# Kernel tuning notes

Hardware: AMD Instinct MI355X
Metric: run time of the kernel (lower is better)

The kernel has to match this reference:

```python
import jax, jax.numpy as jnp
import numpy as np

B, L, D = 1, 1024, 1024
NL = 4            # n_layers
N = 16            # d_state
DI = 2 * D        # d_inner (expand=2)
DTR = (D + 15) // 16  # dt_rank = ceil(d_model/16) = 64
K = 4             # depthwise conv kernel size
EPS = 1e-5


def setup_inputs() -> dict:
    key = jax.random.key(0)
    ks = jax.random.split(key, 8)
    s = lambda k, shp, sc: jax.random.normal(k, shp, jnp.float32) * sc
    x = s(ks[0], (B, L, D), 1.0)
    norm_w = jnp.ones((NL, D), jnp.float32)
    in_w = s(ks[1], (NL, 2 * DI, D), D ** -0.5)          # in_proj (no bias)
    conv_w = s(ks[2], (NL, DI, K), 0.5)                   # depthwise conv1d weight
    conv_b = s(ks[3], (NL, DI), 0.02)                     # conv1d bias
    xproj_w = s(ks[4], (NL, DTR + 2 * N, DI), DI ** -0.5) # x_proj (no bias)
    dt_w = s(ks[5], (NL, DI, DTR), DTR ** -0.5)           # dt_proj weight
    dt_b = jnp.full((NL, DI), 0.1, jnp.float32)           # dt_proj bias (positive-ish delta)
    A_log = jnp.log(jnp.tile(jnp.arange(1, N + 1, dtype=jnp.float32), (NL, DI, 1)))  # [NL, DI, N]
    D_skip = jnp.ones((NL, DI), jnp.float32)
    out_w = s(ks[6], (NL, D, DI), DI ** -0.5)             # out_proj (no bias)
    return dict(x=x, norm_w=norm_w, in_w=in_w, conv_w=conv_w, conv_b=conv_b,
                xproj_w=xproj_w, dt_w=dt_w, dt_b=dt_b, A_log=A_log,
                D_skip=D_skip, out_w=out_w)


def _rmsnorm(x, w):
    return x * jax.lax.rsqrt(jnp.mean(x * x, axis=-1, keepdims=True) + EPS) * w


def _causal_depthwise_conv(u, w, b):
    # u: [B, L, DI], w: [DI, K], b: [DI]; causal (left pad K-1)
    up = jnp.pad(u, ((0, 0), (K - 1, 0), (0, 0)))
    y = b
    for k in range(K):
        y = y + up[:, k:k + L, :] * w[:, k]
    return y


def _selective_scan(dA, dBu, C):
    # dA, dBu: [B, L, DI, N]; C: [B, L, N]
    def step(h, inp):
        a, bu, c = inp
        h = a * h + bu                       # [B, DI, N]
        y = jnp.einsum('bdn,bn->bd', h, c)   # [B, DI]
        return h, y
    h0 = jnp.zeros((dA.shape[0], DI, N), dA.dtype)
    _, ys = jax.lax.scan(step, h0, (dA.transpose(1, 0, 2, 3),
                                    dBu.transpose(1, 0, 2, 3),
                                    C.transpose(1, 0, 2)))
    return ys.transpose(1, 0, 2)             # [B, L, DI]


def _mamba_block(x, p):
    norm_w, in_w, conv_w, conv_b, xproj_w, dt_w, dt_b, A_log, D_skip, out_w = p
    xn = _rmsnorm(x, norm_w)
    xz = jnp.einsum('bld,ed->ble', xn, in_w)             # [B, L, 2*DI]
    u, z = jnp.split(xz, 2, axis=-1)
    u = jax.nn.silu(_causal_depthwise_conv(u, conv_w, conv_b))
    x_dbl = jnp.einsum('bld,ed->ble', u, xproj_w)        # [B, L, DTR+2N]
    dt_r, Bt, Ct = jnp.split(x_dbl, [DTR, DTR + N], axis=-1)
    delta = jax.nn.softplus(jnp.einsum('blr,dr->bld', dt_r, dt_w) + dt_b)  # [B, L, DI]
    A = -jnp.exp(A_log)                                  # [DI, N]
    dA = jnp.exp(delta[..., None] * A)                   # [B, L, DI, N]
    dBu = delta[..., None] * Bt[:, :, None, :] * u[..., None]
    y = _selective_scan(dA, dBu, Ct) + u * D_skip        # [B, L, DI]
    y = y * jax.nn.silu(z)
    return x + jnp.einsum('ble,de->bld', y, out_w)       # residual


def reference(x, norm_w, in_w, conv_w, conv_b, xproj_w, dt_w, dt_b, A_log, D_skip, out_w):
    params = (norm_w, in_w, conv_w, conv_b, xproj_w, dt_w, dt_b, A_log, D_skip, out_w)
    out, _ = jax.lax.scan(lambda h, p: (_mamba_block(h, p), None), x, params)
    return out
```

## Files before the change

### kernel.cpp

```cpp
#include <hip/hip_runtime.h>
#include <hip/hip_bf16.h>
#include <stdint.h>

#define L 1024
#define D 1024
#define NLAYER 4
#define NSTATE 16
#define DI 2048
#define DTR 64
#define KCONV 4
#define XD 96
#define NC 64
#define CT 16
#define KSPLIT 16
#define OSPLIT 4
#define BK 32
#define DIST 4

typedef __attribute__((ext_vector_type(8))) short short8;
typedef __attribute__((ext_vector_type(4))) float floatx4;

__device__ __forceinline__ float siluf(float x) { return x / (1.f + __expf(-x)); }

__device__ __forceinline__ unsigned short f2bf(float x) {
    __hip_bfloat16 b = __float2bfloat16(x);
    return *reinterpret_cast<unsigned short*>(&b);
}

__device__ __forceinline__ short8 pack8(floatx4 a, floatx4 b) {
    short8 o;
    o[0] = (short)f2bf(a.x); o[1] = (short)f2bf(a.y);
    o[2] = (short)f2bf(a.z); o[3] = (short)f2bf(a.w);
    o[4] = (short)f2bf(b.x); o[5] = (short)f2bf(b.y);
    o[6] = (short)f2bf(b.z); o[7] = (short)f2bf(b.w);
    return o;
}

#define BARRIER_NODRAIN() asm volatile("s_waitcnt lgkmcnt(0)\n\ts_barrier" ::: "memory")

template <bool COPYOUT>
__global__ __launch_bounds__(256) void rmsnorm_kernel(const float* __restrict__ x,
                                                      const float* __restrict__ w,
                                                      __hip_bfloat16* __restrict__ xn,
                                                      float* __restrict__ outcpy) {
    int row = blockIdx.x;
    const float* xr = x + (size_t)row * D;
    float v[4];
    float s = 0.f;
#pragma unroll
    for (int i = 0; i < 4; ++i) {
        v[i] = xr[threadIdx.x + i * 256];
        s += v[i] * v[i];
    }
#pragma unroll
    for (int off = 32; off > 0; off >>= 1) s += __shfl_xor(s, off, 64);
    __shared__ float red[4];
    int wave = threadIdx.x >> 6;
    if ((threadIdx.x & 63) == 0) red[wave] = s;
    __syncthreads();
    float tot = red[0] + red[1] + red[2] + red[3];
    float inv = rsqrtf(tot * (1.f / D) + 1e-5f);
#pragma unroll
    for (int i = 0; i < 4; ++i) {
        int c = threadIdx.x + i * 256;
        xn[(size_t)row * D + c] = __float2bfloat16(v[i] * inv * w[c]);
        if (COPYOUT) outcpy[(size_t)row * D + c] = v[i];
    }
}

template <int EPI, int ITERS, bool AF32, int QD>
__global__ __launch_bounds__(256, 2) void gemm_pipe(
    const void* __restrict__ Aptr, int lda,
    const float* __restrict__ Bw, int ldb, int Brows,
    float* __restrict__ C, int ldc, int Nvalid,
    const float* __restrict__ bias) {
    __shared__ __align__(16) __hip_bfloat16 As[2][128 * BK];
    __shared__ __align__(16) __hip_bfloat16 Bs[2][64 * BK];
    int tid = threadIdx.x;
    int wave = tid >> 6, lane = tid & 63;

    int gxy = gridDim.x * gridDim.y;
    int total = gxy * gridDim.z;
    int flat = (blockIdx.z * gridDim.y + blockIdx.y) * gridDim.x + blockIdx.x;
    int bm, bn, bz;
    if ((total & 7) == 0) {
        int lid = (flat & 7) * (total >> 3) + (flat >> 3);
        bz = lid / gxy;
        int rem = lid - bz * gxy;
        bn = rem / gridDim.y;
        bm = rem - bn * gridDim.y;
    } else {
        bm = blockIdx.y; bn = blockIdx.x; bz = blockIdx.z;
    }

    int m0 = bm * 128, n0 = bn * 64;
    int k_base = bz * (ITERS * BK);
    int wr = wave >> 1, wc = wave & 1;
    int srow = lane >> 2, scol = (lane & 3) * 8;
    int q = lane >> 4, r = lane & 15;

    floatx4 acc[4][2] = {};

    int arow0 = m0 + wave * 32 + srow;
    const __hip_bfloat16* gA0 = nullptr; const __hip_bfloat16* gA1 = nullptr;
    const float* gAf0 = nullptr; const float* gAf1 = nullptr;
    if (AF32) {
        gAf0 = (const float*)Aptr + (long)arow0 * lda + scol + k_base;
        gAf1 = gAf0 + (long)16 * lda;
    } else {
        gA0 = (const __hip_bfloat16*)Aptr + (long)arow0 * lda + scol + k_base;
        gA1 = gA0 + (long)16 * lda;
    }
    int bnrow = n0 + wave * 16 + srow;
    const float* gB = Bw + (long)bnrow * ldb + scol + k_base;
    bool bok = bnrow < Brows;

    short8 qa0[QD], qa1[QD];
    floatx4 qaf[AF32 ? QD : 1][4];
    floatx4 qb0[QD] = {}, qb1[QD] = {};

    auto ld = [&](int j) {
        int k0 = j * BK;
        int s = j & (QD - 1);
        if (AF32) {
            qaf[s][0] = *(const floatx4*)(gAf0 + k0);
            qaf[s][1] = *(const floatx4*)(gAf0 + k0 + 4);
            qaf[s][2] = *(const floatx4*)(gAf1 + k0);
            qaf[s][3] = *(const floatx4*)(gAf1 + k0 + 4);
        } else {
            qa0[s] = *(const short8*)(gA0 + k0);
            qa1[s] = *(const short8*)(gA1 + k0);
        }
        if (bok) {
            qb0[s] = *(const floatx4*)(gB + k0);
            qb1[s] = *(const floatx4*)(gB + k0 + 4);
        }
    };
    auto wrstage = [&](int j) {
        int p = j & 1, s = j & (QD - 1);
        if (AF32) {
            *(short8*)(&As[p][(wave * 32 + srow) * BK + scol]) = pack8(qaf[s][0], qaf[s][1]);
            *(short8*)(&As[p][(wave * 32 + 16 + srow) * BK + scol]) = pack8(qaf[s][2], qaf[s][3]);
        } else {
            *(short8*)(&As[p][(wave * 32 + srow) * BK + scol]) = qa0[s];
            *(short8*)(&As[p][(wave * 32 + 16 + srow) * BK + scol]) = qa1[s];
        }
        *(short8*)(&Bs[p][(wave * 16 + srow) * BK + scol]) = pack8(qb0[s], qb1[s]);
    };

#pragma unroll
    for (int j = 0; j < QD; ++j)
        if (j < ITERS) ld(j);
    wrstage(0);

#pragma unroll
    for (int k = 0; k < ITERS; ++k) {
        BARRIER_NODRAIN();
        if (k + QD < ITERS) ld(k + QD);
        if (k + 1 < ITERS) wrstage(k + 1);
        const short* Ap = (const short*)As[k & 1];
        const short* Bp = (const short*)Bs[k & 1];
        short8 af[4], bfr[2];
#pragma unroll
        for (int i = 0; i < 4; ++i)
            af[i] = *(const short8*)(Ap + (wr * 64 + i * 16 + r) * BK + q * 8);
#pragma unroll
        for (int j = 0; j < 2; ++j)
            bfr[j] = *(const short8*)(Bp + (wc * 32 + j * 16 + r) * BK + q * 8);
#pragma unroll
        for (int i = 0; i < 4; ++i)
#pragma unroll
            for (int j = 0; j < 2; ++j)
                acc[i][j] = __builtin_amdgcn_mfma_f32_16x16x32_bf16(af[i], bfr[j], acc[i][j], 0, 0, 0);
    }

#pragma unroll
    for (int i = 0; i < 4; ++i) {
        int mrow = m0 + wr * 64 + i * 16 + q * 4;
#pragma unroll
        for (int j = 0; j < 2; ++j) {
            int ncol = n0 + wc * 32 + j * 16 + r;
            if (ncol < Nvalid) {
#pragma unroll
                for (int rr = 0; rr < 4; ++rr) {
                    float v = acc[i][j][rr];
                    int m = mrow + rr;
                    if (EPI == 1) {
                        v += bias[ncol];
                        v = v > 20.f ? v : log1pf(__expf(v));
                    }
                    if (EPI == 2) atomicAdd(&C[(long)m * ldc + ncol], v);
                    else C[(long)m * ldc + ncol] = v;
                }
            }
        }
    }
}

template <int ITERS, int EPI>
__global__ __launch_bounds__(256, 1) void gemm128(
    const __hip_bfloat16* __restrict__ A, int lda,
    const float* __restrict__ Bw, int ldb, int Brows,
    float* __restrict__ C, int ldc) {
    __shared__ __align__(16) __hip_bfloat16 As[2][128 * BK];
    __shared__ __align__(16) __hip_bfloat16 Bs[2][128 * BK];
    int tid = threadIdx.x;
    int wave = tid >> 6, lane = tid & 63;

    int gxy = gridDim.x * gridDim.y;
    int total = gxy * gridDim.z;
    int flat = (blockIdx.z * gridDim.y + blockIdx.y) * gridDim.x + blockIdx.x;
    int bm, bn, bz;
    if ((total & 7) == 0) {
        int lid = (flat & 7) * (total >> 3) + (flat >> 3);
        bz = lid / gxy;
        int rem = lid - bz * gxy;
        bn = rem / gridDim.y;
        bm = rem - bn * gridDim.y;
    } else {
        bm = blockIdx.y; bn = blockIdx.x; bz = blockIdx.z;
    }

    int m0 = bm * 128, n0 = bn * 128;
    int k_base = bz * (ITERS * BK);
    int wr = wave >> 1, wc = wave & 1;
    int srow = lane >> 2, scol = (lane & 3) * 8;
    int q = lane >> 4, r = lane & 15;

    floatx4 acc[4][4] = {};

    const __hip_bfloat16* gA0 = A + (long)(m0 + wave * 32 + srow) * lda + scol + k_base;
    const __hip_bfloat16* gA1 = gA0 + (long)16 * lda;
    int bn0 = n0 + wave * 32 + srow;
    const float* gB0 = Bw + (long)bn0 * ldb + scol + k_base;
    const float* gB1 = gB0 + (long)16 * ldb;
    bool bok0 = bn0 < Brows, bok1 = (bn0 + 16) < Brows;

    short8 qa0[DIST], qa1[DIST];
    floatx4 qb0[DIST] = {}, qb1[DIST] = {}, qb2[DIST] = {}, qb3[DIST] = {};

    auto ld = [&](int j) {
        int k0 = j * BK;
        int s = j & (DIST - 1);
        qa0[s] = *(const short8*)(gA0 + k0);
        qa1[s] = *(const short8*)(gA1 + k0);
        if (bok0) {
            qb0[s] = *(const floatx4*)(gB0 + k0);
            qb1[s] = *(const floatx4*)(gB0 + k0 + 4);
        }
        if (bok1) {
            qb2[s] = *(const floatx4*)(gB1 + k0);
            qb3[s] = *(const floatx4*)(gB1 + k0 + 4);
        }
    };
    auto wrstage = [&](int j) {
        int p = j & 1, s = j & (DIST - 1);
        *(short8*)(&As[p][(wave * 32 + srow) * BK + scol]) = qa0[s];
        *(short8*)(&As[p][(wave * 32 + 16 + srow) * BK + scol]) = qa1[s];
        *(short8*)(&Bs[p][(wave * 32 + srow) * BK + scol]) = pack8(qb0[s], qb1[s]);
        *(short8*)(&Bs[p][(wave * 32 + 16 + srow) * BK + scol]) = pack8(qb2[s], qb3[s]);
    };

#pragma unroll
    for (int j = 0; j < DIST; ++j)
        if (j < ITERS) ld(j);
    wrstage(0);

#pragma unroll
    for (int k = 0; k < ITERS; ++k) {
        BARRIER_NODRAIN();
        if (k + DIST < ITERS) ld(k + DIST);
        if (k + 1 < ITERS) wrstage(k + 1);
        const short* Ap = (const short*)As[k & 1];
        const short* Bp = (const short*)Bs[k & 1];
        short8 af[4], bfr[4];
#pragma unroll
        for (int i = 0; i < 4; ++i)
            af[i] = *(const short8*)(Ap + (wr * 64 + i * 16 + r) * BK + q * 8);
#pragma unroll
        for (int j = 0; j < 4; ++j)
            bfr[j] = *(const short8*)(Bp + (wc * 64 + j * 16 + r) * BK + q * 8);
#pragma unroll
        for (int i = 0; i < 4; ++i)
#pragma unroll
            for (int j = 0; j < 4; ++j)
                acc[i][j] = __builtin_amdgcn_mfma_f32_16x16x32_bf16(af[i], bfr[j], acc[i][j], 0, 0, 0);
    }

#pragma unroll
    for (int i = 0; i < 4; ++i) {
        int mrow = m0 + wr * 64 + i * 16 + q * 4;
#pragma unroll
        for (int j = 0; j < 4; ++j) {
            int ncol = n0 + wc * 64 + j * 16 + r;
#pragma unroll
            for (int rr = 0; rr < 4; ++rr) {
                if (EPI == 2) atomicAdd(&C[(long)(mrow + rr) * ldc + ncol], acc[i][j][rr]);
                else C[(long)(mrow + rr) * ldc + ncol] = acc[i][j][rr];
            }
        }
    }
}

__global__ __launch_bounds__(256) void conv_silu_kernel(const float* __restrict__ xz,
                                                        const float* __restrict__ cw,
                                                        const float* __restrict__ cb,
                                                        __hip_bfloat16* __restrict__ u,
                                                        float* __restrict__ xdbl96) {
    int idx = blockIdx.x * 256 + threadIdx.x;
    if (blockIdx.x < (L * XD) / 256) xdbl96[idx] = 0.f;
    int d = idx & (DI - 1);
    int t = idx >> 11;
    float acc = cb[d];
#pragma unroll
    for (int k = 0; k < KCONV; ++k) {
        int tk = t - (KCONV - 1) + k;
        if (tk >= 0) acc += xz[(size_t)tk * (2 * DI) + d] * cw[d * KCONV + k];
    }
    u[idx] = __float2bfloat16(siluf(acc));
}

__global__ __launch_bounds__(256) void scanA_kernel(const float* __restrict__ delta,
                                                    const __hip_bfloat16* __restrict__ u,
                                                    const float* __restrict__ xdbl96,
                                                    const float* __restrict__ Alog,
                                                    float* __restrict__ Ach,
                                                    float* __restrict__ Bch) {
    int d = blockIdx.x * 256 + threadIdx.x;
    int c = blockIdx.y;
    __shared__ __align__(16) float Bsh[CT * NSTATE];
    int tt0 = threadIdx.x >> 4, c0 = threadIdx.x & 15;
    Bsh[threadIdx.x] = xdbl96[(size_t)(c * CT + tt0) * XD + DTR + c0];
    __syncthreads();

    float aval[NSTATE];
    const float4* Al4 = (const float4*)(Alog + (size_t)d * NSTATE);
#pragma unroll
    for (int n4 = 0; n4 < 4; ++n4) {
        float4 t = Al4[n4];
        aval[n4 * 4 + 0] = -__expf(t.x);
        aval[n4 * 4 + 1] = -__expf(t.y);
        aval[n4 * 4 + 2] = -__expf(t.z);
        aval[n4 * 4 + 3] = -__expf(t.w);
    }
    float h[NSTATE], ap[NSTATE];
#pragma unroll
    for (int n = 0; n < NSTATE; ++n) { h[n] = 0.f; ap[n] = 1.f; }

    for (int tt = 0; tt < CT; ++tt) {
        int t = c * CT + tt;
        float dl = delta[(size_t)t * DI + d];
        float uu = __bfloat162float(u[(size_t)t * DI + d]);
        float du = dl * uu;
        const float4* Bv = (const float4*)(Bsh + tt * NSTATE);
#pragma unroll
        for (int n4 = 0; n4 < 4; ++n4) {
            float4 b = Bv[n4];
            float bb[4] = {b.x, b.y, b.z, b.w};
#pragma unroll
            for (int k = 0; k < 4; ++k) {
                int n = n4 * 4 + k;
                float a = __expf(dl * aval[n]);
                h[n] = a * h[n] + du * bb[k];
                ap[n] *= a;
            }
        }
    }
    float4* Ao = (float4*)(Ach + ((size_t)c * DI + d) * NSTATE);
    float4* Bo = (float4*)(Bch + ((size_t)c * DI + d) * NSTATE);
#pragma unroll
    for (int n4 = 0; n4 < 4; ++n4) {
        Ao[n4] = make_float4(ap[n4 * 4], ap[n4 * 4 + 1], ap[n4 * 4 + 2], ap[n4 * 4 + 3]);
        Bo[n4] = make_float4(h[n4 * 4], h[n4 * 4 + 1], h[n4 * 4 + 2], h[n4 * 4 + 3]);
    }
}

__global__ __launch_bounds__(256) void scanB_kernel(float* __restrict__ Ach,
                                                    const float* __restrict__ Bch) {
    long i = blockIdx.x * 256 + threadIdx.x;
    const long S = (long)DI * NSTATE;
    constexpr int P = 8;
    float ab[P], bb[P];
#pragma unroll
    for (int j = 0; j < P; ++j) {
        ab[j] = Ach[(long)j * S + i];
        bb[j] = Bch[(long)j * S + i];
    }
    float h = 0.f;
#pragma unroll
    for (int c = 0; c < NC; ++c) {
        float a = ab[c & (P - 1)];
        float b = bb[c & (P - 1)];
        Ach[(long)c * S + i] = h;
        if (c + P < NC) {
            ab[c & (P - 1)] = Ach[(long)(c + P) * S + i];
            bb[c & (P - 1)] = Bch[(long)(c + P) * S + i];
        }
        h = a * h + b;
    }
}

__global__ __launch_bounds__(256) void scanC_kernel(const float* __restrict__ delta,
                                                    const __hip_bfloat16* __restrict__ u,
                                                    const float* __restrict__ xdbl96,
                                                    const float* __restrict__ Alog,
                                                    const float* __restrict__ Hin,
                                                    const float* __restrict__ xz,
                                                    const float* __restrict__ Dskip,
                                                    __hip_bfloat16* __restrict__ yg) {
    int d = blockIdx.x * 256 + threadIdx.x;
    int c = blockIdx.y;
    __shared__ __align__(16) float Bsh[CT * NSTATE];
    __shared__ __align__(16) float Csh[CT * NSTATE];
    int tt0 = threadIdx.x >> 4, c0 = threadIdx.x & 15;
    Bsh[threadIdx.x] = xdbl96[(size_t)(c * CT + tt0) * XD + DTR + c0];
    Csh[threadIdx.x] = xdbl96[(size_t)(c * CT + tt0) * XD + DTR + 16 + c0];
    __syncthreads();

    float aval[NSTATE];
    const float4* Al4 = (const float4*)(Alog + (size_t)d * NSTATE);
#pragma unroll
    for (int n4 = 0; n4 < 4; ++n4) {
        float4 t = Al4[n4];
        aval[n4 * 4 + 0] = -__expf(t.x);
        aval[n4 * 4 + 1] = -__expf(t.y);
        aval[n4 * 4 + 2] = -__expf(t.z);
        aval[n4 * 4 + 3] = -__expf(t.w);
    }
    float h[NSTATE];
    const float4* Hi = (const float4*)(Hin + ((size_t)c * DI + d) * NSTATE);
#pragma unroll
    for (int n4 = 0; n4 < 4; ++n4) {
        float4 t = Hi[n4];
        h[n4 * 4 + 0] = t.x; h[n4 * 4 + 1] = t.y; h[n4 * 4 + 2] = t.z; h[n4 * 4 + 3] = t.w;
    }
    float dsk = Dskip[d];

    for (int tt = 0; tt < CT; ++tt) {
        int t = c * CT + tt;
        float dl = delta[(size_t)t * DI + d];
        float uu = __bfloat162float(u[(size_t)t * DI + d]);
        float du = dl * uu;
        const float4* Bv = (const float4*)(Bsh + tt * NSTATE);
        const float4* Cv = (const float4*)(Csh + tt * NSTATE);
        float y = 0.f;
#pragma unroll
        for (int n4 = 0; n4 < 4; ++n4) {
            float4 b = Bv[n4];
            float4 cc = Cv[n4];
            float bb[4] = {b.x, b.y, b.z, b.w};
            float cv[4] = {cc.x, cc.y, cc.z, cc.w};
#pragma unroll
            for (int k = 0; k < 4; ++k) {
                int n = n4 * 4 + k;
                float a = __expf(dl * aval[n]);
                h[n] = a * h[n] + du * bb[k];
                y += h[n] * cv[k];
            }
        }
        float z = xz[(size_t)t * (2 * DI) + DI + d];
        yg[(size_t)t * DI + d] = __float2bfloat16((y + uu * dsk) * siluf(z));
    }
}

extern "C" void kernel_launch(void* const* d_in, const int* in_sizes, int n_in,
                              void* d_out, int out_size, void* d_ws, size_t ws_size,
                              hipStream_t stream) {
    const float* x      = (const float*)d_in[0];
    const float* norm_w = (const float*)d_in[1];
    const float* in_w   = (const float*)d_in[2];
    const float* conv_w = (const float*)d_in[3];
    const float* conv_b = (const float*)d_in[4];
    const float* xproj_w= (const float*)d_in[5];
    const float* dt_w   = (const float*)d_in[6];
    const float* dt_b   = (const float*)d_in[7];
    const float* A_log  = (const float*)d_in[8];
    const float* D_skip = (const float*)d_in[9];
    const float* out_w  = (const float*)d_in[10];
    float* out = (float*)d_out;

    uint8_t* wp = (uint8_t*)d_ws;
    auto alloc = [&](size_t bytes) {
        uint8_t* p = wp;
        wp += (bytes + 255) & ~(size_t)255;
        return p;
    };
    __hip_bfloat16* xn_bf   = (__hip_bfloat16*)alloc((size_t)L * D * 2);
    float*          xz      = (float*)alloc((size_t)L * 2 * DI * 4);
    __hip_bfloat16* u_bf    = (__hip_bfloat16*)alloc((size_t)L * DI * 2);
    float*          xdbl96  = (float*)alloc((size_t)L * XD * 4);
    float*          delta   = (float*)alloc((size_t)L * DI * 4);
    __hip_bfloat16* yg_bf   = (__hip_bfloat16*)alloc((size_t)L * DI * 2);
    float*          Ach     = (float*)alloc((size_t)NC * DI * NSTATE * 4);
    float*          Bch     = (float*)alloc((size_t)NC * DI * NSTATE * 4);

    rmsnorm_kernel<true><<<L, 256, 0, stream>>>(x, norm_w, xn_bf, out);

    for (int l = 0; l < NLAYER; ++l) {
        gemm128<32, 0><<<dim3(4096 / 128, L / 128, 1), 256, 0, stream>>>(
            xn_bf, D, in_w + (size_t)l * 4096 * 1024, D, 4096, xz, 4096);

        conv_silu_kernel<<<L * DI / 256, 256, 0, stream>>>(
            xz, conv_w + (size_t)l * DI * KCONV, conv_b + (size_t)l * DI, u_bf, xdbl96);

        gemm_pipe<2, 2048 / (KSPLIT * BK), false, 4><<<dim3(2, L / 128, KSPLIT), 256, 0, stream>>>(
            u_bf, DI, xproj_w + (size_t)l * 96 * 2048, DI, 96,
            xdbl96, XD, XD, nullptr);

        gemm_pipe<1, 2, true, 2><<<dim3(2048 / 64, L / 128, 1), 256, 0, stream>>>(
            xdbl96, XD, dt_w + (size_t)l * 2048 * 64, DTR, 2048,
            delta, DI, DI, dt_b + (size_t)l * DI);

        scanA_kernel<<<dim3(DI / 256, NC), 256, 0, stream>>>(
            delta, u_bf, xdbl96, A_log + (size_t)l * DI * NSTATE, Ach, Bch);
        scanB_kernel<<<(DI * NSTATE) / 256, 256, 0, stream>>>(Ach, Bch);
        scanC_kernel<<<dim3(DI / 256, NC), 256, 0, stream>>>(
            delta, u_bf, xdbl96, A_log + (size_t)l * DI * NSTATE, Ach, xz,
            D_skip + (size_t)l * DI, yg_bf);

        gemm128<2048 / (OSPLIT * BK), 2><<<dim3(1024 / 128, L / 128, OSPLIT), 256, 0, stream>>>(
            yg_bf, DI, out_w + (size_t)l * 1024 * 2048, DI, 1024, out, D);

        if (l < NLAYER - 1)
            rmsnorm_kernel<false><<<L, 256, 0, stream>>>(
                out, norm_w + (size_t)(l + 1) * D, xn_bf, nullptr);
    }
}
```

Baseline: 618.4 us.

## Fuse three-pass chunked scan into one kernel with flag sync; deterministic split-K reduce

Replaces the scanA/scanB/scanC launches with a single 512-block kernel that coordinates phases through device-scope flag polling, removing two kernel launches and their drain gaps per layer. It also replaces atomicAdd split-K accumulation in the out-projection with per-split partial buffers, summed in a reduce kernel that also adds the residual and computes the next RMSNorm. The fused scan depends on all 512 blocks being co-resident (launch bounds of 2 per CU), otherwise the spin-waits can deadlock. The reduce adds an extra read of four partial L×D buffers.

```diff
diff --git a/kernel.cpp b/kernel.cpp
--- a/kernel.cpp
+++ b/kernel.cpp
@@ -36,13 +36,38 @@
     return o;
 }
 
+__device__ __forceinline__ void st_dev_u32(uint32_t* p, uint32_t v) {
+    __hip_atomic_store(p, v, __ATOMIC_RELAXED, __HIP_MEMORY_SCOPE_AGENT);
+}
+__device__ __forceinline__ uint32_t ld_dev_u32(const uint32_t* p) {
+    return __hip_atomic_load(p, __ATOMIC_RELAXED, __HIP_MEMORY_SCOPE_AGENT);
+}
+__device__ __forceinline__ void st_dev_u64(void* p, uint64_t v) {
+    __hip_atomic_store((unsigned long long*)p, (unsigned long long)v, __ATOMIC_RELAXED, __HIP_MEMORY_SCOPE_AGENT);
+}
+__device__ __forceinline__ uint64_t ld_dev_u64(const void* p) {
+    return (uint64_t)__hip_atomic_load((const unsigned long long*)p, __ATOMIC_RELAXED, __HIP_MEMORY_SCOPE_AGENT);
+}
+__device__ __forceinline__ float ld_dev_f(const float* p) {
+    uint32_t u = ld_dev_u32((const uint32_t*)p);
+    union { uint32_t u; float f; } c; c.u = u;
+    return c.f;
+}
+__device__ __forceinline__ void st_dev_f(float* p, float v) {
+    union { float f; uint32_t u; } c; c.f = v;
+    st_dev_u32((uint32_t*)p, c.u);
+}
+
 #define BARRIER_NODRAIN() asm volatile("s_waitcnt lgkmcnt(0)\n\ts_barrier" ::: "memory")
 
-template <bool COPYOUT>
 __global__ __launch_bounds__(256) void rmsnorm_kernel(const float* __restrict__ x,
                                                       const float* __restrict__ w,
                                                       __hip_bfloat16* __restrict__ xn,
-                                                      float* __restrict__ outcpy) {
+                                                      uint32_t* __restrict__ flags) {
+    if (blockIdx.x == 0) {
+#pragma unroll
+        for (int i = 0; i < 3; ++i) st_dev_u32(&flags[threadIdx.x + i * 256], 0u);
+    }
     int row = blockIdx.x;
     const float* xr = x + (size_t)row * D;
     float v[4];
@@ -58,13 +83,11 @@
     int wave = threadIdx.x >> 6;
     if ((threadIdx.x & 63) == 0) red[wave] = s;
     __syncthreads();
-    float tot = red[0] + red[1] + red[2] + red[3];
-    float inv = rsqrtf(tot * (1.f / D) + 1e-5f);
+    float inv = rsqrtf((red[0] + red[1] + red[2] + red[3]) * (1.f / D) + 1e-5f);
 #pragma unroll
     for (int i = 0; i < 4; ++i) {
         int c = threadIdx.x + i * 256;
         xn[(size_t)row * D + c] = __float2bfloat16(v[i] * inv * w[c]);
-        if (COPYOUT) outcpy[(size_t)row * D + c] = v[i];
     }
 }
 
@@ -197,11 +220,11 @@
     }
 }
 
-template <int ITERS, int EPI>
+template <int ITERS>
 __global__ __launch_bounds__(256, 1) void gemm128(
     const __hip_bfloat16* __restrict__ A, int lda,
     const float* __restrict__ Bw, int ldb, int Brows,
-    float* __restrict__ C, int ldc) {
+    float* __restrict__ C, int ldc, long zstride) {
     __shared__ __align__(16) __hip_bfloat16 As[2][128 * BK];
     __shared__ __align__(16) __hip_bfloat16 Bs[2][128 * BK];
     int tid = threadIdx.x;
@@ -223,6 +246,7 @@
 
     int m0 = bm * 128, n0 = bn * 128;
     int k_base = bz * (ITERS * BK);
+    C += (long)bz * zstride;
     int wr = wave >> 1, wc = wave & 1;
     int srow = lane >> 2, scol = (lane & 3) * 8;
     int q = lane >> 4, r = lane & 15;
@@ -294,10 +318,45 @@
         for (int j = 0; j < 4; ++j) {
             int ncol = n0 + wc * 64 + j * 16 + r;
 #pragma unroll
-            for (int rr = 0; rr < 4; ++rr) {
-                if (EPI == 2) atomicAdd(&C[(long)(mrow + rr) * ldc + ncol], acc[i][j][rr]);
-                else C[(long)(mrow + rr) * ldc + ncol] = acc[i][j][rr];
-            }
+            for (int rr = 0; rr < 4; ++rr)
+                C[(long)(mrow + rr) * ldc + ncol] = acc[i][j][rr];
+        }
+    }
+}
+
+template <int NPART, bool NORM>
+__global__ __launch_bounds__(256) void reduce_kernel(const float* __restrict__ part2,
+                                                     const float* __restrict__ xin,
+                                                     const float* __restrict__ nw,
+                                                     float* __restrict__ out,
+                                                     __hip_bfloat16* __restrict__ xn) {
+    int row = blockIdx.x;
+    const float* xr = xin + (size_t)row * D;
+    float v[4];
+    float ss = 0.f;
+#pragma unroll
+    for (int i = 0; i < 4; ++i) {
+        int c = threadIdx.x + i * 256;
+        float s = xr[c];
+#pragma unroll
+        for (int p = 0; p < NPART; ++p)
+            s += part2[(size_t)p * L * D + (size_t)row * D + c];
+        v[i] = s;
+        out[(size_t)row * D + c] = s;
+        ss += s * s;
+    }
+    if (NORM) {
+#pragma unroll
+        for (int off = 32; off > 0; off >>= 1) ss += __shfl_xor(ss, off, 64);
+        __shared__ float red[4];
+        int wave = threadIdx.x >> 6;
+        if ((threadIdx.x & 63) == 0) red[wave] = ss;
+        __syncthreads();
+        float inv = rsqrtf((red[0] + red[1] + red[2] + red[3]) * (1.f / D) + 1e-5f);
+#pragma unroll
+        for (int i = 0; i < 4; ++i) {
+            int c = threadIdx.x + i * 256;
+            xn[(size_t)row * D + c] = __float2bfloat16(v[i] * inv * nw[c]);
         }
     }
 }
@@ -320,146 +379,149 @@
     u[idx] = __float2bfloat16(siluf(acc));
 }
 
-__global__ __launch_bounds__(256) void scanA_kernel(const float* __restrict__ delta,
-                                                    const __hip_bfloat16* __restrict__ u,
-                                                    const float* __restrict__ xdbl96,
-                                                    const float* __restrict__ Alog,
-                                                    float* __restrict__ Ach,
-                                                    float* __restrict__ Bch) {
-    int d = blockIdx.x * 256 + threadIdx.x;
-    int c = blockIdx.y;
-    __shared__ __align__(16) float Bsh[CT * NSTATE];
-    int tt0 = threadIdx.x >> 4, c0 = threadIdx.x & 15;
-    Bsh[threadIdx.x] = xdbl96[(size_t)(c * CT + tt0) * XD + DTR + c0];
-    __syncthreads();
-
-    float aval[NSTATE];
-    const float4* Al4 = (const float4*)(Alog + (size_t)d * NSTATE);
-#pragma unroll
-    for (int n4 = 0; n4 < 4; ++n4) {
-        float4 t = Al4[n4];
-        aval[n4 * 4 + 0] = -__expf(t.x);
-        aval[n4 * 4 + 1] = -__expf(t.y);
-        aval[n4 * 4 + 2] = -__expf(t.z);
-        aval[n4 * 4 + 3] = -__expf(t.w);
-    }
-    float h[NSTATE], ap[NSTATE];
-#pragma unroll
-    for (int n = 0; n < NSTATE; ++n) { h[n] = 0.f; ap[n] = 1.f; }
-
-    for (int tt = 0; tt < CT; ++tt) {
-        int t = c * CT + tt;
-        float dl = delta[(size_t)t * DI + d];
-        float uu = __bfloat162float(u[(size_t)t * DI + d]);
-        float du = dl * uu;
-        const float4* Bv = (const float4*)(Bsh + tt * NSTATE);
-#pragma unroll
-        for (int n4 = 0; n4 < 4; ++n4) {
-            float4 b = Bv[n4];
-            float bb[4] = {b.x, b.y, b.z, b.w};
-#pragma unroll
-            for (int k = 0; k < 4; ++k) {
-                int n = n4 * 4 + k;
-                float a = __expf(dl * aval[n]);
-                h[n] = a * h[n] + du * bb[k];
-                ap[n] *= a;
-            }
-        }
-    }
-    float4* Ao = (float4*)(Ach + ((size_t)c * DI + d) * NSTATE);
-    float4* Bo = (float4*)(Bch + ((size_t)c * DI + d) * NSTATE);
-#pragma unroll
-    for (int n4 = 0; n4 < 4; ++n4) {
-        Ao[n4] = make_float4(ap[n4 * 4], ap[n4 * 4 + 1], ap[n4 * 4 + 2], ap[n4 * 4 + 3]);
-        Bo[n4] = make_float4(h[n4 * 4], h[n4 * 4 + 1], h[n4 * 4 + 2], h[n4 * 4 + 3]);
-    }
-}
-
-__global__ __launch_bounds__(256) void scanB_kernel(float* __restrict__ Ach,
-                                                    const float* __restrict__ Bch) {
-    long i = blockIdx.x * 256 + threadIdx.x;
-    const long S = (long)DI * NSTATE;
-    constexpr int P = 8;
-    float ab[P], bb[P];
-#pragma unroll
-    for (int j = 0; j < P; ++j) {
-        ab[j] = Ach[(long)j * S + i];
-        bb[j] = Bch[(long)j * S + i];
-    }
-    float h = 0.f;
-#pragma unroll
-    for (int c = 0; c < NC; ++c) {
-        float a = ab[c & (P - 1)];
-        float b = bb[c & (P - 1)];
-        Ach[(long)c * S + i] = h;
-        if (c + P < NC) {
-            ab[c & (P - 1)] = Ach[(long)(c + P) * S + i];
-            bb[c & (P - 1)] = Bch[(long)(c + P) * S + i];
-        }
-        h = a * h + b;
-    }
-}
-
-__global__ __launch_bounds__(256) void scanC_kernel(const float* __restrict__ delta,
-                                                    const __hip_bfloat16* __restrict__ u,
-                                                    const float* __restrict__ xdbl96,
-                                                    const float* __restrict__ Alog,
-                                                    const float* __restrict__ Hin,
-                                                    const float* __restrict__ xz,
-                                                    const float* __restrict__ Dskip,
-                                                    __hip_bfloat16* __restrict__ yg) {
-    int d = blockIdx.x * 256 + threadIdx.x;
-    int c = blockIdx.y;
+__global__ __launch_bounds__(256, 2) void scan_fused(
+    const float* __restrict__ delta, const __hip_bfloat16* __restrict__ u,
+    const float* __restrict__ xdbl96, const float* __restrict__ Alog,
+    const float* __restrict__ xz, const float* __restrict__ Dskip,
+    float* __restrict__ Ach, float* __restrict__ Bch,
+    __hip_bfloat16* __restrict__ yg,
+    uint32_t* __restrict__ flagsA, uint32_t* __restrict__ flagsB, int layer) {
+    const int bid = blockIdx.x, tid = threadIdx.x;
+    const int g = bid & 7, c = bid >> 3;
+    const int d = g * 256 + tid;
+    const uint32_t tgt = (uint32_t)(layer + 1);
     __shared__ __align__(16) float Bsh[CT * NSTATE];
     __shared__ __align__(16) float Csh[CT * NSTATE];
-    int tt0 = threadIdx.x >> 4, c0 = threadIdx.x & 15;
-    Bsh[threadIdx.x] = xdbl96[(size_t)(c * CT + tt0) * XD + DTR + c0];
-    Csh[threadIdx.x] = xdbl96[(size_t)(c * CT + tt0) * XD + DTR + 16 + c0];
-    __syncthreads();
 
     float aval[NSTATE];
-    const float4* Al4 = (const float4*)(Alog + (size_t)d * NSTATE);
-#pragma unroll
-    for (int n4 = 0; n4 < 4; ++n4) {
-        float4 t = Al4[n4];
-        aval[n4 * 4 + 0] = -__expf(t.x);
-        aval[n4 * 4 + 1] = -__expf(t.y);
-        aval[n4 * 4 + 2] = -__expf(t.z);
-        aval[n4 * 4 + 3] = -__expf(t.w);
-    }
-    float h[NSTATE];
-    const float4* Hi = (const float4*)(Hin + ((size_t)c * DI + d) * NSTATE);
-#pragma unroll
-    for (int n4 = 0; n4 < 4; ++n4) {
-        float4 t = Hi[n4];
-        h[n4 * 4 + 0] = t.x; h[n4 * 4 + 1] = t.y; h[n4 * 4 + 2] = t.z; h[n4 * 4 + 3] = t.w;
-    }
-    float dsk = Dskip[d];
-
-    for (int tt = 0; tt < CT; ++tt) {
-        int t = c * CT + tt;
-        float dl = delta[(size_t)t * DI + d];
-        float uu = __bfloat162float(u[(size_t)t * DI + d]);
-        float du = dl * uu;
-        const float4* Bv = (const float4*)(Bsh + tt * NSTATE);
-        const float4* Cv = (const float4*)(Csh + tt * NSTATE);
-        float y = 0.f;
+    {
+        const floatx4* Al4 = (const floatx4*)(Alog + (size_t)d * NSTATE);
 #pragma unroll
         for (int n4 = 0; n4 < 4; ++n4) {
-            float4 b = Bv[n4];
-            float4 cc = Cv[n4];
-            float bb[4] = {b.x, b.y, b.z, b.w};
-            float cv[4] = {cc.x, cc.y, cc.z, cc.w};
-#pragma unroll
-            for (int k = 0; k < 4; ++k) {
-                int n = n4 * 4 + k;
-                float a = __expf(dl * aval[n]);
-                h[n] = a * h[n] + du * bb[k];
-                y += h[n] * cv[k];
+            floatx4 t = Al4[n4];
+            aval[n4 * 4 + 0] = -__expf(t[0]);
+            aval[n4 * 4 + 1] = -__expf(t[1]);
+            aval[n4 * 4 + 2] = -__expf(t[2]);
+            aval[n4 * 4 + 3] = -__expf(t[3]);
+        }
+    }
+
+    {
+        Bsh[tid] = xdbl96[(size_t)(c * CT + (tid >> 4)) * XD + DTR + (tid & 15)];
+        __syncthreads();
+        float h[NSTATE], ap[NSTATE];
+#pragma unroll
+        for (int n = 0; n < NSTATE; ++n) { h[n] = 0.f; ap[n] = 1.f; }
+        for (int tt = 0; tt < CT; ++tt) {
+            int t = c * CT + tt;
+            float dl = delta[(size_t)t * DI + d];
+            float uu = __bfloat162float(u[(size_t)t * DI + d]);
+            float du = dl * uu;
+            const floatx4* Bv = (const floatx4*)(Bsh + tt * NSTATE);
+#pragma unroll
+            for (int n4 = 0; n4 < 4; ++n4) {
+                floatx4 b = Bv[n4];
+#pragma unroll
+                for (int k = 0; k < 4; ++k) {
+                    int n = n4 * 4 + k;
+                    float a = __expf(dl * aval[n]);
+                    h[n] = a * h[n] + du * b[k];
+                    ap[n] *= a;
+                }
             }
         }
-        float z = xz[(size_t)t * (2 * DI) + DI + d];
-        yg[(size_t)t * DI + d] = __float2bfloat16((y + uu * dsk) * siluf(z));
+        float* Ao = Ach + ((size_t)c * DI + d) * NSTATE;
+        float* Bo = Bch + ((size_t)c * DI + d) * NSTATE;
+#pragma unroll
+        for (int n2 = 0; n2 < 8; ++n2) {
+            union { float f[2]; uint64_t u; } ca, cb2;
+            ca.f[0] = ap[n2 * 2]; ca.f[1] = ap[n2 * 2 + 1];
+            cb2.f[0] = h[n2 * 2]; cb2.f[1] = h[n2 * 2 + 1];
+            st_dev_u64(Ao + n2 * 2, ca.u);
+            st_dev_u64(Bo + n2 * 2, cb2.u);
+        }
+        asm volatile("s_waitcnt vmcnt(0)" ::: "memory");
+        __syncthreads();
+        if (tid == 0) st_dev_u32(&flagsA[c * 8 + g], tgt);
+    }
+
+    if (bid < 128) {
+        int gb = bid >> 4;
+        if (tid < 64) {
+            while (ld_dev_u32(&flagsA[tid * 8 + gb]) < tgt)
+                __builtin_amdgcn_s_sleep(8);
+        }
+        __syncthreads();
+        long i = (long)bid * 256 + tid;
+        const long S = (long)DI * NSTATE;
+        constexpr int P = 8;
+        float ab[P], bb[P];
+#pragma unroll
+        for (int j = 0; j < P; ++j) {
+            ab[j] = ld_dev_f(Ach + (long)j * S + i);
+            bb[j] = ld_dev_f(Bch + (long)j * S + i);
+        }
+        float h = 0.f;
+#pragma unroll
+        for (int cc = 0; cc < NC; ++cc) {
+            float a = ab[cc & (P - 1)];
+            float b = bb[cc & (P - 1)];
+            st_dev_f(Ach + (long)cc * S + i, h);
+            if (cc + P < NC) {
+                ab[cc & (P - 1)] = ld_dev_f(Ach + (long)(cc + P) * S + i);
+                bb[cc & (P - 1)] = ld_dev_f(Bch + (long)(cc + P) * S + i);
+            }
+            h = a * h + b;
+        }
+        asm volatile("s_waitcnt vmcnt(0)" ::: "memory");
+        __syncthreads();
+        if (tid == 0) st_dev_u32(&flagsB[bid], tgt);
+    }
+
+    {
+        if (tid < 16) {
+            while (ld_dev_u32(&flagsB[g * 16 + tid]) < tgt)
+                __builtin_amdgcn_s_sleep(8);
+        }
+        __syncthreads();
+        Bsh[tid] = xdbl96[(size_t)(c * CT + (tid >> 4)) * XD + DTR + (tid & 15)];
+        Csh[tid] = xdbl96[(size_t)(c * CT + (tid >> 4)) * XD + DTR + 16 + (tid & 15)];
+        __syncthreads();
+
+        float h[NSTATE];
+        {
+            const float* Hi = Ach + ((size_t)c * DI + d) * NSTATE;
+#pragma unroll
+            for (int n2 = 0; n2 < 8; ++n2) {
+                union { uint64_t u; float f[2]; } cv;
+                cv.u = ld_dev_u64(Hi + n2 * 2);
+                h[n2 * 2] = cv.f[0]; h[n2 * 2 + 1] = cv.f[1];
+            }
+        }
+        float dsk = Dskip[d];
+        for (int tt = 0; tt < CT; ++tt) {
+            int t = c * CT + tt;
+            float dl = delta[(size_t)t * DI + d];
+            float uu = __bfloat162float(u[(size_t)t * DI + d]);
+            float du = dl * uu;
+            const floatx4* Bv = (const floatx4*)(Bsh + tt * NSTATE);
+            const floatx4* Cv = (const floatx4*)(Csh + tt * NSTATE);
+            float y = 0.f;
+#pragma unroll
+            for (int n4 = 0; n4 < 4; ++n4) {
+                floatx4 b = Bv[n4];
+                floatx4 cc = Cv[n4];
+#pragma unroll
+                for (int k = 0; k < 4; ++k) {
+                    int n = n4 * 4 + k;
+                    float a = __expf(dl * aval[n]);
+                    h[n] = a * h[n] + du * b[k];
+                    y += h[n] * cc[k];
+                }
+            }
+            float z = xz[(size_t)t * (2 * DI) + DI + d];
+            yg[(size_t)t * DI + d] = __float2bfloat16((y + uu * dsk) * siluf(z));
+        }
     }
 }
 
@@ -491,14 +553,18 @@
     float*          xdbl96  = (float*)alloc((size_t)L * XD * 4);
     float*          delta   = (float*)alloc((size_t)L * DI * 4);
     __hip_bfloat16* yg_bf   = (__hip_bfloat16*)alloc((size_t)L * DI * 2);
+    float*          part2   = (float*)alloc((size_t)OSPLIT * L * D * 4);
     float*          Ach     = (float*)alloc((size_t)NC * DI * NSTATE * 4);
     float*          Bch     = (float*)alloc((size_t)NC * DI * NSTATE * 4);
-
-    rmsnorm_kernel<true><<<L, 256, 0, stream>>>(x, norm_w, xn_bf, out);
+    uint32_t*       flags   = (uint32_t*)alloc(768 * 4);
+
+    rmsnorm_kernel<<<L, 256, 0, stream>>>(x, norm_w, xn_bf, flags);
 
     for (int l = 0; l < NLAYER; ++l) {
-        gemm128<32, 0><<<dim3(4096 / 128, L / 128, 1), 256, 0, stream>>>(
-            xn_bf, D, in_w + (size_t)l * 4096 * 1024, D, 4096, xz, 4096);
+        const float* xin = (l == 0) ? x : out;
+
+        gemm128<32><<<dim3(4096 / 128, L / 128, 1), 256, 0, stream>>>(
+            xn_bf, D, in_w + (size_t)l * 4096 * 1024, D, 4096, xz, 4096, 0);
 
         conv_silu_kernel<<<L * DI / 256, 256, 0, stream>>>(
             xz, conv_w + (size_t)l * DI * KCONV, conv_b + (size_t)l * DI, u_bf, xdbl96);
@@ -511,18 +577,19 @@
             xdbl96, XD, dt_w + (size_t)l * 2048 * 64, DTR, 2048,
             delta, DI, DI, dt_b + (size_t)l * DI);
 
-        scanA_kernel<<<dim3(DI / 256, NC), 256, 0, stream>>>(
-            delta, u_bf, xdbl96, A_log + (size_t)l * DI * NSTATE, Ach, Bch);
-        scanB_kernel<<<(DI * NSTATE) / 256, 256, 0, stream>>>(Ach, Bch);
-        scanC_kernel<<<dim3(DI / 256, NC), 256, 0, stream>>>(
-            delta, u_bf, xdbl96, A_log + (size_t)l * DI * NSTATE, Ach, xz,
-            D_skip + (size_t)l * DI, yg_bf);
-
-        gemm128<2048 / (OSPLIT * BK), 2><<<dim3(1024 / 128, L / 128, OSPLIT), 256, 0, stream>>>(
-            yg_bf, DI, out_w + (size_t)l * 1024 * 2048, DI, 1024, out, D);
+        scan_fused<<<512, 256, 0, stream>>>(
+            delta, u_bf, xdbl96, A_log + (size_t)l * DI * NSTATE, xz,
+            D_skip + (size_t)l * DI, Ach, Bch, yg_bf, flags, flags + 512, l);
+
+        gemm128<2048 / (OSPLIT * BK)><<<dim3(1024 / 128, L / 128, OSPLIT), 256, 0, stream>>>(
+            yg_bf, DI, out_w + (size_t)l * 1024 * 2048, DI, 1024,
+            part2, D, (long)L * D);
 
         if (l < NLAYER - 1)
-            rmsnorm_kernel<false><<<L, 256, 0, stream>>>(
-                out, norm_w + (size_t)(l + 1) * D, xn_bf, nullptr);
-    }
-}
+            reduce_kernel<OSPLIT, true><<<L, 256, 0, stream>>>(
+                part2, xin, norm_w + (size_t)(l + 1) * D, out, xn_bf);
+        else
+            reduce_kernel<OSPLIT, false><<<L, 256, 0, stream>>>(
+                part2, xin, nullptr, out, nullptr);
+    }
+}
```

New measurement: 742.3 us. +20.0%, slower.
